# Kernel tuning notes

Hardware: AMD Instinct MI355X
Metric: run time of the kernel (lower is better)

## Reference

```python
import jax, jax.numpy as jnp
import numpy as np

B, DM, H, W = 2, 96, 48, 48
E = 192          # d_expand == d_inner
R, N = 6, 16     # delta_rank, d_state


def conv2d(x, w, b, groups=1, pad=0):
    out = jax.lax.conv_general_dilated(
        x, w, window_strides=(1, 1), padding=[(pad, pad), (pad, pad)],
        dimension_numbers=("NCHW", "OIHW", "NCHW"), feature_group_count=groups)
    return out + b[None, :, None, None]


def setup_inputs() -> dict:
    key = jax.random.key(0)
    ks = jax.random.split(key, 24)
    f = lambda k, shape, s: jax.random.normal(k, shape, jnp.float32) * s
    inp = {
        "x": jax.random.normal(ks[0], (B, DM, H, W), jnp.float32),
        "in_proj_w": f(ks[1], (2 * E, DM), 0.05),
        "conv_w": f(ks[2], (E, 1, 3, 3), 0.2),
        "conv_b": f(ks[3], (E,), 0.1),
        "x_proj_w": f(ks[4], (4, R + 2 * N, E), 0.01),
        "dt_proj_w": f(ks[5], (4, E, R), 0.01),
        "dt_proj_b": jnp.full((4, E), -9.0) + f(ks[6], (4, E), 0.1),
        "A_log": jnp.tile(jnp.log(jnp.arange(1, N + 1, dtype=jnp.float32))[None, None, :], (4, E, 1)),
        "Ds": jnp.ones((4, E), jnp.float32),
        "ln_g": jnp.ones(E, jnp.float32), "ln_b": jnp.zeros(E, jnp.float32),
        "c1_w": f(ks[7], (2 * E, E, 1, 1), 0.05), "c1_b": jnp.zeros(2 * E),
        "bn1_g": jnp.ones(2 * E), "bn1_b": jnp.zeros(2 * E), "bn1_m": jnp.zeros(2 * E), "bn1_v": jnp.ones(2 * E),
        "c2_w": f(ks[8], (2 * E, 1, 3, 3), 0.2), "c2_b": jnp.zeros(2 * E),
        "bn2_g": jnp.ones(2 * E), "bn2_b": jnp.zeros(2 * E), "bn2_m": jnp.zeros(2 * E), "bn2_v": jnp.ones(2 * E),
        "c3_w": f(ks[9], (E // 2, 2 * E, 1, 1), 0.05), "c3_b": jnp.zeros(E // 2),
        "se1_w": f(ks[10], (E // 4, E // 2), 0.1), "se1_b": jnp.zeros(E // 4),
        "se2_w": f(ks[11], (E // 2, E // 4), 0.1), "se2_b": jnp.zeros(E // 2),
    }
    return inp


def reference(x, in_proj_w, conv_w, conv_b, x_proj_w, dt_proj_w, dt_proj_b,
              A_log, Ds, ln_g, ln_b,
              c1_w, c1_b, bn1_g, bn1_b, bn1_m, bn1_v,
              c2_w, c2_b, bn2_g, bn2_b, bn2_m, bn2_v,
              c3_w, c3_b, se1_w, se1_b, se2_w, se2_b):
    Bs, _, Hs, Ws = x.shape
    L = Hs * Ws
    # in projection (Linear over channel dim), split x/z gates
    xz = jnp.einsum("bchw,oc->bohw", x, in_proj_w)
    xi, z = jnp.split(xz, 2, axis=1)
    # depthwise conv + SiLU
    xi = jax.nn.silu(conv2d(xi, conv_w, conv_b, groups=E, pad=1))
    # ---- selective scan (4-direction cross scan, cumsum formulation) ----
    xf = xi.reshape(Bs, E, L)
    xt = jnp.swapaxes(xi, 2, 3).reshape(Bs, E, L)
    xs = jnp.stack([xf, xf[..., ::-1], xt, xt[..., ::-1]], axis=1)  # [B,4,E,L]
    dbc = jnp.einsum("bkcl,krc->bkrl", xs, x_proj_w)                # [B,4,R+2N,L]
    dlt, b, c = dbc[:, :, :R], dbc[:, :, R:R + N], dbc[:, :, R + N:]
    dlt = jnp.einsum("bkrl,kdr->bkdl", dlt, dt_proj_w) + dt_proj_b[None, :, :, None]
    dlt = jax.nn.softplus(dlt)                                      # [B,4,E,L]
    dA = dlt[..., None] * A_log[None, :, :, None, :]                # [B,4,E,L,N]
    phi = jnp.exp(-jnp.cumsum(dA, axis=3))
    dbx = dlt[..., None] * jnp.swapaxes(b, 2, 3)[:, :, None] * xs[..., None]  # [B,4,E,L,N]
    h = phi * jnp.cumsum(dbx / (phi + 1e-12), axis=3)
    y = jnp.einsum("bkdln,bknl->bkdl", h, c) + Ds[None, :, :, None]  # [B,4,E,L]
    # ---- cross merge ----
    y1 = y[:, 0]
    y2 = y[:, 1, :, ::-1]
    y3 = jnp.swapaxes(y[:, 2].reshape(Bs, E, Ws, Hs), 2, 3).reshape(Bs, E, L)
    y4 = jnp.swapaxes(y[:, 3, :, ::-1].reshape(Bs, E, Ws, Hs), 2, 3).reshape(Bs, E, L)
    ys = (y1 + y2 + y3 + y4).reshape(Bs, E, Hs, Ws)
    # layernorm over channels
    yn = jnp.moveaxis(ys, 1, -1)
    mu = yn.mean(-1, keepdims=True)
    var = yn.var(-1, keepdims=True)
    yn = (yn - mu) / jnp.sqrt(var + 1e-5) * ln_g + ln_b
    u = jnp.moveaxis(yn, -1, 1) * z
    # ---- EFFN ----
    def bn(t, g, bb, m, v):
        return (t - m[None, :, None, None]) / jnp.sqrt(v + 1e-5)[None, :, None, None] * g[None, :, None, None] + bb[None, :, None, None]
    t = jax.nn.relu(bn(conv2d(u, c1_w, c1_b), bn1_g, bn1_b, bn1_m, bn1_v))
    t = jax.nn.relu(bn(conv2d(t, c2_w, c2_b, groups=2 * E, pad=1), bn2_g, bn2_b, bn2_m, bn2_v))
    t = conv2d(t, c3_w, c3_b)
    # squeeze-excitation: t + t * sigmoid(fc(relu(fc(avgpool(t)))))
    s = t.mean((2, 3))
    s = jax.nn.relu(s @ se1_w.T + se1_b)
    s = jax.nn.sigmoid(s @ se2_w.T + se2_b)
    return t + t * s[:, :, None, None]
```

## Files before the change

kernel.cpp:

```cpp
#include <hip/hip_runtime.h>
#include <hip/hip_bf16.h>

#define LTOT 2304
#define ECH  192
#define NCH  16
#define CCH  192
#define SCH  12

__device__ __forceinline__ int permS(int k, int l) {
  if (k == 0) return l;
  if (k == 1) return LTOT - 1 - l;
  int m = (k == 2) ? l : (LTOT - 1 - l);
  return (m % 48) * 48 + (m / 48);
}

__device__ __forceinline__ float sp_fast(float x) {
  float t = __expf(x);
  return (t <= 0.018f) ? t * fmaf(t, fmaf(t, 0.33333334f, -0.5f), 1.f) : log1pf(t);
}

__global__ __launch_bounds__(256) void k1_inproj(const float* __restrict__ x,
                                                 const float* __restrict__ W,
                                                 float* __restrict__ xi_pre,
                                                 float* __restrict__ z) {
  const int l0 = blockIdx.x * 32;
  const int o0 = blockIdx.y * 64;
  const int b  = blockIdx.z;
  __shared__ __align__(16) float xs[96 * 34];
  __shared__ __align__(16) float Wl[96 * 68];
  const int tid = threadIdx.x;
  for (int idx = tid; idx < 96 * 32; idx += 256) {
    int i = idx & 31, cc = idx >> 5;
    xs[cc * 34 + i] = x[(b * 96 + cc) * LTOT + l0 + i];
  }
  for (int idx = tid; idx < 64 * 96; idx += 256) {
    int r = idx / 96, cc = idx - r * 96;
    Wl[cc * 68 + r] = W[(o0 + r) * 96 + cc];
  }
  __syncthreads();
  const int lane = tid & 63, w = tid >> 6;
  const int jj = lane & 15, rqq = lane >> 4;
  const int rbase = 16 * w + 4 * rqq;
  float acc[2][4];
#pragma unroll
  for (int p = 0; p < 2; ++p)
#pragma unroll
    for (int t = 0; t < 4; ++t) acc[p][t] = 0.f;
#pragma unroll 4
  for (int cc = 0; cc < 96; ++cc) {
    const float4 wv = *(const float4*)&Wl[cc * 68 + rbase];
    const float2 xv = *(const float2*)&xs[cc * 34 + 2 * jj];
    acc[0][0] = fmaf(wv.x, xv.x, acc[0][0]); acc[0][1] = fmaf(wv.y, xv.x, acc[0][1]);
    acc[0][2] = fmaf(wv.z, xv.x, acc[0][2]); acc[0][3] = fmaf(wv.w, xv.x, acc[0][3]);
    acc[1][0] = fmaf(wv.x, xv.y, acc[1][0]); acc[1][1] = fmaf(wv.y, xv.y, acc[1][1]);
    acc[1][2] = fmaf(wv.z, xv.y, acc[1][2]); acc[1][3] = fmaf(wv.w, xv.y, acc[1][3]);
  }
  __syncthreads();
  float* ol = xs;
#pragma unroll
  for (int t = 0; t < 4; ++t) {
    ol[(rbase + t) * 33 + 2 * jj]     = acc[0][t];
    ol[(rbase + t) * 33 + 2 * jj + 1] = acc[1][t];
  }
  __syncthreads();
  for (int idx = tid; idx < 32 * 64; idx += 256) {
    int r = idx & 63, pos = idx >> 6;
    float v = ol[r * 33 + pos];
    int o = o0 + r, l = l0 + pos;
    if (o < ECH) xi_pre[(b * LTOT + l) * ECH + o] = v;
    else         z[(b * LTOT + l) * ECH + (o - ECH)] = v;
  }
}

__global__ __launch_bounds__(256) void k2_dwconv(const float* __restrict__ xi_pre,
                                                 const float* __restrict__ cw,
                                                 const float* __restrict__ cb,
                                                 float* __restrict__ xi) {
  int g = blockIdx.x * 256 + threadIdx.x;
  if (g >= 2 * LTOT * ECH) return;
  int e = g % ECH; int l = (g / ECH) % LTOT; int b = g / (ECH * LTOT);
  int h = l / 48, wq = l % 48;
  float acc = cb[e];
#pragma unroll
  for (int kh = 0; kh < 3; ++kh) {
    int hh = h + kh - 1; if (hh < 0 || hh >= 48) continue;
#pragma unroll
    for (int kw = 0; kw < 3; ++kw) {
      int ww = wq + kw - 1; if (ww < 0 || ww >= 48) continue;
      acc = fmaf(cw[e * 9 + kh * 3 + kw], xi_pre[(b * LTOT + hh * 48 + ww) * ECH + e], acc);
    }
  }
  xi[g] = acc / (1.f + __expf(-acc));
}

__global__ __launch_bounds__(256) void k3_xproj(const float* __restrict__ xi,
                                                const float* __restrict__ xw,
                                                float* __restrict__ dl6g,
                                                float* __restrict__ bT,
                                                float* __restrict__ cT) {
  const int l0 = blockIdx.x * 32;
  const int k  = blockIdx.y;
  const int b  = blockIdx.z;
  __shared__ __align__(16) float xs[96 * 34];
  __shared__ __align__(16) float Wl[192 * 40];
  const int tid = threadIdx.x;
  const float* wsrc = xw + k * 38 * ECH;
  for (int idx = tid; idx < 38 * 192; idx += 256) {
    int r = idx / 192, cc = idx - r * 192;
    Wl[cc * 40 + r] = wsrc[idx];
  }
  const int lane = tid & 63, w = tid >> 6;
  const int jj = lane & 15;
  const int rq = w * 4 + (lane >> 4);
  const int rqc = rq < 9 ? rq : 9;
  const int j0 = 2 * jj;
  float a00 = 0.f, a01 = 0.f, a02 = 0.f, a03 = 0.f;
  float a10 = 0.f, a11 = 0.f, a12 = 0.f, a13 = 0.f;
  for (int kc = 0; kc < 2; ++kc) {
    __syncthreads();
    for (int idx = tid; idx < 32 * 96; idx += 256) {
      int j = idx / 96, cc = idx - j * 96;
      int s = permS(k, l0 + j);
      xs[cc * 34 + j] = xi[(b * LTOT + s) * ECH + kc * 96 + cc];
    }
    __syncthreads();
#pragma unroll 4
    for (int cc = 0; cc < 96; ++cc) {
      const float2 xv = *(const float2*)&xs[cc * 34 + j0];
      const float4 wv = *(const float4*)&Wl[(kc * 96 + cc) * 40 + 4 * rqc];
      a00 = fmaf(wv.x, xv.x, a00); a01 = fmaf(wv.y, xv.x, a01);
      a02 = fmaf(wv.z, xv.x, a02); a03 = fmaf(wv.w, xv.x, a03);
      a10 = fmaf(wv.x, xv.y, a10); a11 = fmaf(wv.y, xv.y, a11);
      a12 = fmaf(wv.z, xv.y, a12); a13 = fmaf(wv.w, xv.y, a13);
    }
  }
  const int bk = b * 4 + k;
  if (rq < 10) {
    float av[2][4] = {{a00, a01, a02, a03}, {a10, a11, a12, a13}};
#pragma unroll
    for (int t = 0; t < 4; ++t) {
      int r = 4 * rq + t;
      if (r >= 38) continue;
#pragma unroll
      for (int p = 0; p < 2; ++p) {
        int j = j0 + p;
        float v = av[p][t];
        if (r < 6)       dl6g[((bk * LTOT) + l0 + j) * 6 + r] = v;
        else if (r < 22) bT[((bk * LTOT) + l0 + j) * NCH + (r - 6)] = v;
        else             cT[((bk * LTOT) + l0 + j) * NCH + (r - 22)] = v;
      }
    }
  }
}

__global__ __launch_bounds__(256) void k4a_scan1(const float* __restrict__ dl6g,
                                                 const float* __restrict__ xi,
                                                 const float* __restrict__ bT,
                                                 const float* __restrict__ Alog,
                                                 const float* __restrict__ dtw,
                                                 const float* __restrict__ dtb,
                                                 float* __restrict__ q,
                                                 float* __restrict__ Ts) {
  const int cb = blockIdx.x;
  const int db = blockIdx.y;
  const int bk = blockIdx.z;
  const int b = bk >> 2, k = bk & 3;
  const int l0 = cb * 48;
  __shared__ __align__(16) float2 sdx[48 * 64];
  __shared__ __align__(16) float  sb[48 * NCH];
  const int tid = threadIdx.x;
  const int dd = tid & 63, cg = tid >> 6;
  const int dg = db * 64 + dd;
  float b6 = dtb[k * ECH + dg];
  float w6[6];
  {
    const float2* d2 = (const float2*)(dtw + (k * ECH + dg) * 6);
    float2 u0 = d2[0], u1 = d2[1], u2 = d2[2];
    w6[0] = u0.x; w6[1] = u0.y; w6[2] = u1.x; w6[3] = u1.y; w6[4] = u2.x; w6[5] = u2.y;
  }
  for (int idx = tid; idx < 48 * NCH; idx += 256) sb[idx] = bT[(bk * LTOT + l0) * NCH + idx];
  for (int e = tid; e < 48 * 64; e += 256) {
    int s = e >> 6;
    const float* d6 = dl6g + (bk * LTOT + l0 + s) * 6;
    float xa = b6;
#pragma unroll
    for (int r = 0; r < 6; ++r) xa = fmaf(w6[r], d6[r], xa);
    float dl = sp_fast(xa);
    int sp = permS(k, l0 + s);
    sdx[s * 64 + dd] = make_float2(dl, xi[(b * LTOT + sp) * ECH + dg]);
  }
  float C1[16], h[16];
#pragma unroll
  for (int n = 0; n < 16; ++n) {
    C1[n] = Alog[(k * ECH + dg) * NCH + n];
    h[n] = 0.f;
  }
  __syncthreads();
  float Tsum = 0.f;
  for (int i = 0; i < SCH; ++i) {
    int j = cg * SCH + i;
    float2 dx = sdx[j * 64 + dd];
    float dl = dx.x;
    float u  = dl * dx.y;
    Tsum += dl;
    const float4* bb4 = (const float4*)(sb + j * NCH);
    float4 q0 = bb4[0], q1 = bb4[1], q2 = bb4[2], q3 = bb4[3];
    float bbl[16] = {q0.x, q0.y, q0.z, q0.w, q1.x, q1.y, q1.z, q1.w,
                     q2.x, q2.y, q2.z, q2.w, q3.x, q3.y, q3.z, q3.w};
    if (dl <= 0.018f) {
#pragma unroll
      for (int n = 0; n < 16; ++n) {
        float xn = C1[n] * dl;
        float e = fmaf(xn, fmaf(xn, fmaf(xn, -(1.f / 6.f), 0.5f), -1.f), 1.f);
        h[n] = fmaf(e, h[n], u * bbl[n]);
      }
    } else {
#pragma unroll
      for (int n = 0; n < 16; ++n) {
        float e = __expf(-C1[n] * dl);
        h[n] = fmaf(e, h[n], u * bbl[n]);
      }
    }
  }
  const int c = cb * 4 + cg;
  float4* qp = (float4*)(q + ((bk * CCH + c) * ECH + dg) * NCH);
  qp[0] = make_float4(h[0], h[1], h[2], h[3]);
  qp[1] = make_float4(h[4], h[5], h[6], h[7]);
  qp[2] = make_float4(h[8], h[9], h[10], h[11]);
  qp[3] = make_float4(h[12], h[13], h[14], h[15]);
  Ts[(bk * CCH + c) * ECH + dg] = Tsum;
}

__global__ __launch_bounds__(256) void k4b_comb(const float* __restrict__ Alog,
                                                const float* __restrict__ Ts,
                                                float* __restrict__ q) {
  const int d  = blockIdx.x;
  const int bk = blockIdx.y;
  const int k  = bk & 3;
  const int tid = threadIdx.x;
  const int n = tid & 15, seg = tid >> 4;
  const float A = Alog[(k * ECH + d) * NCH + n];
  const int c0 = seg * 12;
  const float* tb = Ts + (bk * CCH + c0) * ECH + d;
  float* qp = q + ((bk * CCH + c0) * ECH + d) * NCH + n;
  float qv[12], P[12];
#pragma unroll
  for (int i = 0; i < 12; ++i) qv[i] = qp[i * (ECH * NCH)];
#pragma unroll
  for (int i = 0; i < 12; ++i) {
    float xv = A * tb[i * ECH];
    P[i] = (xv <= 0.05f)
               ? fmaf(xv, fmaf(xv, fmaf(xv, -(1.f / 6.f), 0.5f), -1.f), 1.f)
               : __expf(-xv);
  }
  float hl = 0.f, Pp = 1.f;
#pragma unroll
  for (int i = 0; i < 12; ++i) { hl = fmaf(P[i], hl, qv[i]); Pp *= P[i]; }
  __shared__ float2 comb[16][17];
  comb[seg][n] = make_float2(Pp, hl);
  __syncthreads();
  float H = 0.f;
  for (int s = 0; s < seg; ++s) {
    float2 cb = comb[s][n];
    H = fmaf(cb.x, H, cb.y);
  }
  float h = H;
#pragma unroll
  for (int i = 0; i < 12; ++i) {
    float hp = h;
    h = fmaf(P[i], h, qv[i]);
    qp[i * (ECH * NCH)] = hp;
  }
}

__global__ __launch_bounds__(256) void k4c_scan2(const float* __restrict__ dl6g,
                                                 const float* __restrict__ xi,
                                                 const float* __restrict__ bT,
                                                 const float* __restrict__ cT,
                                                 const float* __restrict__ Alog,
                                                 const float* __restrict__ dtw,
                                                 const float* __restrict__ dtb,
                                                 const float* __restrict__ hin,
                                                 float* __restrict__ yd) {
  const int cb = blockIdx.x;
  const int db = blockIdx.y;
  const int bk = blockIdx.z;
  const int b = bk >> 2, k = bk & 3;
  const int l0 = cb * 48;
  __shared__ __align__(16) float2 sdx[48 * 64];
  __shared__ __align__(16) float  sb[48 * NCH];
  __shared__ __align__(16) float  sc[48 * NCH];
  const int tid = threadIdx.x;
  const int dd = tid & 63, cg = tid >> 6;
  const int dg = db * 64 + dd;
  float b6 = dtb[k * ECH + dg];
  float w6[6];
  {
    const float2* d2 = (const float2*)(dtw + (k * ECH + dg) * 6);
    float2 u0 = d2[0], u1 = d2[1], u2 = d2[2];
    w6[0] = u0.x; w6[1] = u0.y; w6[2] = u1.x; w6[3] = u1.y; w6[4] = u2.x; w6[5] = u2.y;
  }
  for (int idx = tid; idx < 48 * NCH; idx += 256) {
    sb[idx] = bT[(bk * LTOT + l0) * NCH + idx];
    sc[idx] = cT[(bk * LTOT + l0) * NCH + idx];
  }
  for (int e = tid; e < 48 * 64; e += 256) {
    int s = e >> 6;
    const float* d6 = dl6g + (bk * LTOT + l0 + s) * 6;
    float xa = b6;
#pragma unroll
    for (int r = 0; r < 6; ++r) xa = fmaf(w6[r], d6[r], xa);
    float dl = sp_fast(xa);
    int sp = permS(k, l0 + s);
    sdx[s * 64 + dd] = make_float2(dl, xi[(b * LTOT + sp) * ECH + dg]);
  }
  float C1[16], h[16];
  const int c = cb * 4 + cg;
  const float4* hp = (const float4*)(hin + ((bk * CCH + c) * ECH + dg) * NCH);
  {
    float4 h0 = hp[0], h1 = hp[1], h2 = hp[2], h3 = hp[3];
    h[0]=h0.x; h[1]=h0.y; h[2]=h0.z; h[3]=h0.w;
    h[4]=h1.x; h[5]=h1.y; h[6]=h1.z; h[7]=h1.w;
    h[8]=h2.x; h[9]=h2.y; h[10]=h2.z; h[11]=h2.w;
    h[12]=h3.x; h[13]=h3.y; h[14]=h3.z; h[15]=h3.w;
  }
#pragma unroll
  for (int n = 0; n < 16; ++n) C1[n] = Alog[(k * ECH + dg) * NCH + n];
  float* ydk = yd + (b * 4 + k) * LTOT * ECH;
  __syncthreads();
  for (int i = 0; i < SCH; ++i) {
    int j = cg * SCH + i;
    float2 dx = sdx[j * 64 + dd];
    float dl = dx.x;
    float u  = dl * dx.y;
    const float4* bb4 = (const float4*)(sb + j * NCH);
    float4 q0 = bb4[0], q1 = bb4[1], q2 = bb4[2], q3 = bb4[3];
    float bbl[16] = {q0.x, q0.y, q0.z, q0.w, q1.x, q1.y, q1.z, q1.w,
                     q2.x, q2.y, q2.z, q2.w, q3.x, q3.y, q3.z, q3.w};
    if (dl <= 0.018f) {
#pragma unroll
      for (int n = 0; n < 16; ++n) {
        float xn = C1[n] * dl;
        float e = fmaf(xn, fmaf(xn, fmaf(xn, -(1.f / 6.f), 0.5f), -1.f), 1.f);
        h[n] = fmaf(e, h[n], u * bbl[n]);
      }
    } else {
#pragma unroll
      for (int n = 0; n < 16; ++n) {
        float e = __expf(-C1[n] * dl);
        h[n] = fmaf(e, h[n], u * bbl[n]);
      }
    }
    const float4* cc4 = (const float4*)(sc + j * NCH);
    float4 c0 = cc4[0], c1 = cc4[1], c2 = cc4[2], c3 = cc4[3];
    float ccl[16] = {c0.x, c0.y, c0.z, c0.w, c1.x, c1.y, c1.z, c1.w,
                     c2.x, c2.y, c2.z, c2.w, c3.x, c3.y, c3.z, c3.w};
    float y = 0.f;
#pragma unroll
    for (int n = 0; n < 16; ++n) y = fmaf(h[n], ccl[n], y);
    int sp = permS(k, l0 + j);
    ydk[sp * ECH + dg] = y;
  }
}

__global__ __launch_bounds__(256) void k5_ln(const float* __restrict__ yd,
                                             const float* __restrict__ Ds,
                                             const float* __restrict__ lng,
                                             const float* __restrict__ lnb,
                                             float* __restrict__ zu) {
  int p = blockIdx.x * 4 + (threadIdx.x >> 6);
  int lane = threadIdx.x & 63;
  int b = (p >= LTOT) ? 1 : 0;
  int l = p - b * LTOT;
  const float* y0 = yd + (b * 4) * LTOT * ECH + l * ECH;
  float vd[3], sd[3];
#pragma unroll
  for (int t = 0; t < 3; ++t) {
    int d = lane + t * 64;
    vd[t] = ((y0[d] + y0[LTOT * ECH + d]) + y0[2 * LTOT * ECH + d]) + y0[3 * LTOT * ECH + d];
    sd[t] = Ds[d] + Ds[ECH + d] + Ds[2 * ECH + d] + Ds[3 * ECH + d];
  }
  float s1 = vd[0] + vd[1] + vd[2];
  float s2 = sd[0] + sd[1] + sd[2];
#pragma unroll
  for (int off = 32; off > 0; off >>= 1) {
    s1 += __shfl_xor(s1, off, 64);
    s2 += __shfl_xor(s2, off, 64);
  }
  float mean_dot = s1 * (1.f / 192.f);
  float mean_sd  = s2 * (1.f / 192.f);
  float dev[3];
  float ss = 0.f;
#pragma unroll
  for (int t = 0; t < 3; ++t) {
    dev[t] = (vd[t] - mean_dot) + (sd[t] - mean_sd);
    ss = fmaf(dev[t], dev[t], ss);
  }
#pragma unroll
  for (int off = 32; off > 0; off >>= 1) ss += __shfl_xor(ss, off, 64);
  float rstd = 1.f / sqrtf(ss * (1.f / 192.f) + 1e-5f);
#pragma unroll
  for (int t = 0; t < 3; ++t) {
    int d = lane + t * 64;
    float yn = (dev[t] * rstd) * lng[d] + lnb[d];
    zu[p * ECH + d] = yn * zu[p * ECH + d];
  }
}

__global__ __launch_bounds__(256) void k6_c1(const float* __restrict__ u,
                                             const float* __restrict__ W,
                                             const float* __restrict__ c1b,
                                             const float* __restrict__ g1,
                                             const float* __restrict__ b1,
                                             const float* __restrict__ m1,
                                             const float* __restrict__ v1,
                                             float* __restrict__ t1,
                                             float* __restrict__ se) {
  const int l0 = blockIdx.x * 32;
  const int o0 = blockIdx.y * 64;
  const int b  = blockIdx.z;
  const int tid = threadIdx.x;
  if (blockIdx.x == 0 && blockIdx.y == 0 && blockIdx.z == 0 && tid < 192) se[tid] = 0.f;
  __shared__ __align__(16) float xs[96 * 34];
  __shared__ __align__(16) float Wl[96 * 68];
  const int lane = tid & 63, w = tid >> 6;
  const int jj = lane & 15, rqq = lane >> 4;
  const int rbase = 16 * w + 4 * rqq;
  float acc[2][4];
#pragma unroll
  for (int p = 0; p < 2; ++p)
#pragma unroll
    for (int t = 0; t < 4; ++t) acc[p][t] = 0.f;
  for (int kc = 0; kc < 2; ++kc) {
    if (kc) __syncthreads();
    for (int idx = tid; idx < 32 * 96; idx += 256) {
      int cc = idx % 96, i = idx / 96;
      xs[cc * 34 + i] = u[(b * LTOT + l0 + i) * ECH + kc * 96 + cc];
    }
    for (int idx = tid; idx < 64 * 96; idx += 256) {
      int r = idx / 96, cc = idx - r * 96;
      Wl[cc * 68 + r] = W[(o0 + r) * ECH + kc * 96 + cc];
    }
    __syncthreads();
#pragma unroll 4
    for (int cc = 0; cc < 96; ++cc) {
      const float4 wv = *(const float4*)&Wl[cc * 68 + rbase];
      const float2 xv = *(const float2*)&xs[cc * 34 + 2 * jj];
      acc[0][0] = fmaf(wv.x, xv.x, acc[0][0]); acc[0][1] = fmaf(wv.y, xv.x, acc[0][1]);
      acc[0][2] = fmaf(wv.z, xv.x, acc[0][2]); acc[0][3] = fmaf(wv.w, xv.x, acc[0][3]);
      acc[1][0] = fmaf(wv.x, xv.y, acc[1][0]); acc[1][1] = fmaf(wv.y, xv.y, acc[1][1]);
      acc[1][2] = fmaf(wv.z, xv.y, acc[1][2]); acc[1][3] = fmaf(wv.w, xv.y, acc[1][3]);
    }
  }
#pragma unroll
  for (int t = 0; t < 4; ++t) {
    int o = o0 + rbase + t;
    float sc = g1[o] / sqrtf(v1[o] + 1e-5f);
    float bias = (c1b[o] - m1[o]) * sc + b1[o];
#pragma unroll
    for (int p = 0; p < 2; ++p) acc[p][t] = fmaxf(fmaf(acc[p][t], sc, bias), 0.f);
  }
  __syncthreads();
  float* ol = xs;
#pragma unroll
  for (int t = 0; t < 4; ++t) {
    ol[(rbase + t) * 33 + 2 * jj]     = acc[0][t];
    ol[(rbase + t) * 33 + 2 * jj + 1] = acc[1][t];
  }
  __syncthreads();
  for (int idx = tid; idx < 32 * 64; idx += 256) {
    int pos = idx & 31, r = idx >> 5;
    t1[(b * 384 + o0 + r) * LTOT + l0 + pos] = ol[r * 33 + pos];
  }
}

__global__ __launch_bounds__(256) void k7_dw2(const float* __restrict__ t1,
                                              const float* __restrict__ cw,
                                              const float* __restrict__ cb,
                                              const float* __restrict__ g2,
                                              const float* __restrict__ b2,
                                              const float* __restrict__ m2,
                                              const float* __restrict__ v2,
                                              float* __restrict__ t2) {
  int g = blockIdx.x * 256 + threadIdx.x;
  if (g >= 2 * LTOT * 384) return;
  int l = g % LTOT; int o = (g / LTOT) % 384; int b = g / (LTOT * 384);
  int h = l / 48, wq = l % 48;
  const float* src = t1 + (b * 384 + o) * LTOT;
  float acc = cb[o];
#pragma unroll
  for (int kh = 0; kh < 3; ++kh) {
    int hh = h + kh - 1; if (hh < 0 || hh >= 48) continue;
#pragma unroll
    for (int kw = 0; kw < 3; ++kw) {
      int ww = wq + kw - 1; if (ww < 0 || ww >= 48) continue;
      acc = fmaf(cw[o * 9 + kh * 3 + kw], src[hh * 48 + ww], acc);
    }
  }
  float sc = g2[o] / sqrtf(v2[o] + 1e-5f);
  float val = (acc - m2[o]) * sc + b2[o];
  t2[g] = fmaxf(val, 0.f);
}

__global__ __launch_bounds__(256) void k8_c3(const float* __restrict__ t2,
                                             const float* __restrict__ W,
                                             const float* __restrict__ c3b,
                                             float* __restrict__ t3,
                                             float* __restrict__ se) {
  const int l0 = blockIdx.x * 32;
  const int r0 = blockIdx.y * 32;
  const int b  = blockIdx.z;
  __shared__ __align__(16) float Wl[384 * 34];
  __shared__ __align__(16) float xs[192 * 34];
  const int tid = threadIdx.x;
  const int lane = tid & 63, w = tid >> 6;
  const int jj = lane & 15, rqq = lane >> 4;
  const int rloc = 8 * w + 2 * rqq;
  for (int idx = tid; idx < 32 * 384; idx += 256) {
    int r = idx / 384, cc = idx - r * 384;
    Wl[cc * 34 + r] = W[(r0 + r) * 384 + cc];
  }
  float acc[2][2];
  acc[0][0] = acc[0][1] = acc[1][0] = acc[1][1] = 0.f;
  for (int kc = 0; kc < 2; ++kc) {
    if (kc) __syncthreads();
    for (int idx = tid; idx < 192 * 32; idx += 256) {
      int i = idx & 31, cc = idx >> 5;
      xs[cc * 34 + i] = t2[(b * 384 + kc * 192 + cc) * LTOT + l0 + i];
    }
    __syncthreads();
#pragma unroll 4
    for (int cc = 0; cc < 192; ++cc) {
      const float2 wv = *(const float2*)&Wl[(kc * 192 + cc) * 34 + rloc];
      const float2 xv = *(const float2*)&xs[cc * 34 + 2 * jj];
      acc[0][0] = fmaf(wv.x, xv.x, acc[0][0]); acc[0][1] = fmaf(wv.y, xv.x, acc[0][1]);
      acc[1][0] = fmaf(wv.x, xv.y, acc[1][0]); acc[1][1] = fmaf(wv.y, xv.y, acc[1][1]);
    }
  }
  {
    float b0 = c3b[r0 + rloc], b1v = c3b[r0 + rloc + 1];
    acc[0][0] += b0; acc[1][0] += b0; acc[0][1] += b1v; acc[1][1] += b1v;
  }
#pragma unroll
  for (int t = 0; t < 2; ++t) {
    float v = acc[0][t] + acc[1][t];
    v += __shfl_xor(v, 1); v += __shfl_xor(v, 2);
    v += __shfl_xor(v, 4); v += __shfl_xor(v, 8);
    if (jj == 0) atomicAdd(&se[b * 96 + r0 + rloc + t], v);
  }
  __syncthreads();
  float* ol = xs;
#pragma unroll
  for (int t = 0; t < 2; ++t) {
    ol[(rloc + t) * 33 + 2 * jj]     = acc[0][t];
    ol[(rloc + t) * 33 + 2 * jj + 1] = acc[1][t];
  }
  __syncthreads();
  for (int idx = tid; idx < 32 * 32; idx += 256) {
    int pos = idx & 31, r = idx >> 5;
    t3[(b * 96 + r0 + r) * LTOT + l0 + pos] = ol[r * 33 + pos];
  }
}

__global__ __launch_bounds__(256) void k9_out(const float* __restrict__ t3,
                                              const float* __restrict__ se,
                                              const float* __restrict__ w1,
                                              const float* __restrict__ sb1,
                                              const float* __restrict__ w2,
                                              const float* __restrict__ sb2,
                                              float* __restrict__ out) {
  __shared__ float sm[192];
  __shared__ float s1[96];
  __shared__ float smul[192];
  int t = threadIdx.x;
  if (t < 192) sm[t] = se[t] * (1.f / 2304.f);
  __syncthreads();
  if (t < 96) {
    int b = t / 48, i = t % 48;
    float a = sb1[i];
#pragma unroll 4
    for (int m = 0; m < 96; ++m) a = fmaf(w1[i * 96 + m], sm[b * 96 + m], a);
    s1[t] = fmaxf(a, 0.f);
  }
  __syncthreads();
  if (t < 192) {
    int b = t / 96, j = t % 96;
    float a = sb2[j];
#pragma unroll 4
    for (int i = 0; i < 48; ++i) a = fmaf(w2[j * 48 + i], s1[b * 48 + i], a);
    smul[t] = 1.f + 1.f / (1.f + __expf(-a));
  }
  __syncthreads();
  int g = blockIdx.x * 256 + t;
  if (g < 2 * 96 * LTOT) out[g] = t3[g] * smul[g / LTOT];
}

extern "C" void kernel_launch(void* const* d_in, const int* in_sizes, int n_in,
                              void* d_out, int out_size, void* d_ws, size_t ws_size,
                              hipStream_t stream) {
  const float* x     = (const float*)d_in[0];
  const float* inw   = (const float*)d_in[1];
  const float* convw = (const float*)d_in[2];
  const float* convb = (const float*)d_in[3];
  const float* xpw   = (const float*)d_in[4];
  const float* dtw   = (const float*)d_in[5];
  const float* dtb   = (const float*)d_in[6];
  const float* Alog  = (const float*)d_in[7];
  const float* Ds    = (const float*)d_in[8];
  const float* lng   = (const float*)d_in[9];
  const float* lnb   = (const float*)d_in[10];
  const float* c1w   = (const float*)d_in[11];
  const float* c1b   = (const float*)d_in[12];
  const float* bn1g  = (const float*)d_in[13];
  const float* bn1b  = (const float*)d_in[14];
  const float* bn1m  = (const float*)d_in[15];
  const float* bn1v  = (const float*)d_in[16];
  const float* c2w   = (const float*)d_in[17];
  const float* c2b   = (const float*)d_in[18];
  const float* bn2g  = (const float*)d_in[19];
  const float* bn2b  = (const float*)d_in[20];
  const float* bn2m  = (const float*)d_in[21];
  const float* bn2v  = (const float*)d_in[22];
  const float* c3w   = (const float*)d_in[23];
  const float* c3b   = (const float*)d_in[24];
  const float* se1w  = (const float*)d_in[25];
  const float* se1b  = (const float*)d_in[26];
  const float* se2w  = (const float*)d_in[27];
  const float* se2b  = (const float*)d_in[28];

  float* ws = (float*)d_ws;
  float* xi_pre = ws;
  float* z      = ws + 884736;
  float* xi     = ws + 1769472;
  float* dl6g   = ws + 2654208;
  float* bT     = ws + 2764800;
  float* cT     = ws + 3354624;
  float* q      = ws + 3944448;
  float* Ts     = ws + 13381632;
  float* se     = ws + 13676544;
  float* yd     = ws + 13676736;
  float* t1 = yd;
  float* t2 = yd + 1769472;
  float* t3 = q;

  k1_inproj<<<dim3(72, 6, 2), 256, 0, stream>>>(x, inw, xi_pre, z);
  k2_dwconv<<<3456, 256, 0, stream>>>(xi_pre, convw, convb, xi);
  k3_xproj<<<dim3(72, 4, 2), 256, 0, stream>>>(xi, xpw, dl6g, bT, cT);
  k4a_scan1<<<dim3(48, 3, 8), 256, 0, stream>>>(dl6g, xi, bT, Alog, dtw, dtb, q, Ts);
  k4b_comb<<<dim3(192, 8), 256, 0, stream>>>(Alog, Ts, q);
  k4c_scan2<<<dim3(48, 3, 8), 256, 0, stream>>>(dl6g, xi, bT, cT, Alog, dtw, dtb, q, yd);
  k5_ln<<<1152, 256, 0, stream>>>(yd, Ds, lng, lnb, z);
  k6_c1<<<dim3(72, 6, 2), 256, 0, stream>>>(z, c1w, c1b, bn1g, bn1b, bn1m, bn1v, t1, se);
  k7_dw2<<<6912, 256, 0, stream>>>(t1, c2w, c2b, bn2g, bn2b, bn2m, bn2v, t2);
  k8_c3<<<dim3(72, 3, 2), 256, 0, stream>>>(t2, c3w, c3b, t3, se);
  k9_out<<<1728, 256, 0, stream>>>(t3, se, se1w, se1b, se2w, se2b, (float*)d_out);
}
```

Baseline: 301.0 us.

## Vectorize dwconvs, atomically merge scan directions, and premultiply delta*x in scan

The change makes the depthwise convolutions in k2 and k7 compute four outputs per thread with float4 loads and stores, with the weights hoisted into registers. k4c now accumulates the four scan directions into one zeroed buffer through atomicAdd, so k5 reads one tensor instead of four, at the cost of atomic traffic plus an extra memset. It also precomputes delta*x when staging to shared memory, vectorizes the weight transpose loads in k1 and k6, and pads k3's weight stride in shared memory. The atomic float adds make the summation order nondeterministic, and the workspace aliases for t1, t2 and t3 are moved into the q region.

```diff
diff --git a/kernel.cpp b/kernel.cpp
--- a/kernel.cpp
+++ b/kernel.cpp
@@ -33,9 +33,14 @@
     int i = idx & 31, cc = idx >> 5;
     xs[cc * 34 + i] = x[(b * 96 + cc) * LTOT + l0 + i];
   }
-  for (int idx = tid; idx < 64 * 96; idx += 256) {
-    int r = idx / 96, cc = idx - r * 96;
-    Wl[cc * 68 + r] = W[(o0 + r) * 96 + cc];
+  for (int idx = tid; idx < 96 * 16; idx += 256) {
+    int cc = idx % 96, rq = idx / 96;
+    float4 v;
+    v.x = W[(o0 + 4 * rq + 0) * 96 + cc];
+    v.y = W[(o0 + 4 * rq + 1) * 96 + cc];
+    v.z = W[(o0 + 4 * rq + 2) * 96 + cc];
+    v.w = W[(o0 + 4 * rq + 3) * 96 + cc];
+    *(float4*)&Wl[cc * 68 + 4 * rq] = v;
   }
   __syncthreads();
   const int lane = tid & 63, w = tid >> 6;
@@ -72,25 +77,40 @@
   }
 }
 
-__global__ __launch_bounds__(256) void k2_dwconv(const float* __restrict__ xi_pre,
+__global__ __launch_bounds__(256) void k2_dwconv(const float4* __restrict__ xi_pre4,
                                                  const float* __restrict__ cw,
                                                  const float* __restrict__ cb,
-                                                 float* __restrict__ xi) {
+                                                 float4* __restrict__ xi4) {
   int g = blockIdx.x * 256 + threadIdx.x;
-  if (g >= 2 * LTOT * ECH) return;
-  int e = g % ECH; int l = (g / ECH) % LTOT; int b = g / (ECH * LTOT);
+  if (g >= 2 * LTOT * 48) return;
+  int e4 = g % 48; int l = (g / 48) % LTOT; int b = g / (48 * LTOT);
   int h = l / 48, wq = l % 48;
-  float acc = cb[e];
+  int e0 = 4 * e4;
+  float wt[4][9];
+#pragma unroll
+  for (int j = 0; j < 4; ++j)
+#pragma unroll
+    for (int t = 0; t < 9; ++t) wt[j][t] = cw[(e0 + j) * 9 + t];
+  float4 acc = *(const float4*)&cb[e0];
 #pragma unroll
   for (int kh = 0; kh < 3; ++kh) {
     int hh = h + kh - 1; if (hh < 0 || hh >= 48) continue;
 #pragma unroll
     for (int kw = 0; kw < 3; ++kw) {
       int ww = wq + kw - 1; if (ww < 0 || ww >= 48) continue;
-      acc = fmaf(cw[e * 9 + kh * 3 + kw], xi_pre[(b * LTOT + hh * 48 + ww) * ECH + e], acc);
-    }
-  }
-  xi[g] = acc / (1.f + __expf(-acc));
+      float4 v = xi_pre4[(b * LTOT + hh * 48 + ww) * 48 + e4];
+      int t = kh * 3 + kw;
+      acc.x = fmaf(wt[0][t], v.x, acc.x);
+      acc.y = fmaf(wt[1][t], v.y, acc.y);
+      acc.z = fmaf(wt[2][t], v.z, acc.z);
+      acc.w = fmaf(wt[3][t], v.w, acc.w);
+    }
+  }
+  acc.x = acc.x / (1.f + __expf(-acc.x));
+  acc.y = acc.y / (1.f + __expf(-acc.y));
+  acc.z = acc.z / (1.f + __expf(-acc.z));
+  acc.w = acc.w / (1.f + __expf(-acc.w));
+  xi4[g] = acc;
 }
 
 __global__ __launch_bounds__(256) void k3_xproj(const float* __restrict__ xi,
@@ -102,12 +122,12 @@
   const int k  = blockIdx.y;
   const int b  = blockIdx.z;
   __shared__ __align__(16) float xs[96 * 34];
-  __shared__ __align__(16) float Wl[192 * 40];
+  __shared__ __align__(16) float Wl[192 * 44];
   const int tid = threadIdx.x;
   const float* wsrc = xw + k * 38 * ECH;
   for (int idx = tid; idx < 38 * 192; idx += 256) {
     int r = idx / 192, cc = idx - r * 192;
-    Wl[cc * 40 + r] = wsrc[idx];
+    Wl[cc * 44 + r] = wsrc[idx];
   }
   const int lane = tid & 63, w = tid >> 6;
   const int jj = lane & 15;
@@ -127,7 +147,7 @@
 #pragma unroll 4
     for (int cc = 0; cc < 96; ++cc) {
       const float2 xv = *(const float2*)&xs[cc * 34 + j0];
-      const float4 wv = *(const float4*)&Wl[(kc * 96 + cc) * 40 + 4 * rqc];
+      const float4 wv = *(const float4*)&Wl[(kc * 96 + cc) * 44 + 4 * rqc];
       a00 = fmaf(wv.x, xv.x, a00); a01 = fmaf(wv.y, xv.x, a01);
       a02 = fmaf(wv.z, xv.x, a02); a03 = fmaf(wv.w, xv.x, a03);
       a10 = fmaf(wv.x, xv.y, a10); a11 = fmaf(wv.y, xv.y, a11);
@@ -187,7 +207,7 @@
     for (int r = 0; r < 6; ++r) xa = fmaf(w6[r], d6[r], xa);
     float dl = sp_fast(xa);
     int sp = permS(k, l0 + s);
-    sdx[s * 64 + dd] = make_float2(dl, xi[(b * LTOT + sp) * ECH + dg]);
+    sdx[s * 64 + dd] = make_float2(dl, dl * xi[(b * LTOT + sp) * ECH + dg]);
   }
   float C1[16], h[16];
 #pragma unroll
@@ -201,7 +221,7 @@
     int j = cg * SCH + i;
     float2 dx = sdx[j * 64 + dd];
     float dl = dx.x;
-    float u  = dl * dx.y;
+    float u  = dx.y;
     Tsum += dl;
     const float4* bb4 = (const float4*)(sb + j * NCH);
     float4 q0 = bb4[0], q1 = bb4[1], q2 = bb4[2], q3 = bb4[3];
@@ -281,7 +301,7 @@
                                                  const float* __restrict__ dtw,
                                                  const float* __restrict__ dtb,
                                                  const float* __restrict__ hin,
-                                                 float* __restrict__ yd) {
+                                                 float* __restrict__ ys) {
   const int cb = blockIdx.x;
   const int db = blockIdx.y;
   const int bk = blockIdx.z;
@@ -312,7 +332,7 @@
     for (int r = 0; r < 6; ++r) xa = fmaf(w6[r], d6[r], xa);
     float dl = sp_fast(xa);
     int sp = permS(k, l0 + s);
-    sdx[s * 64 + dd] = make_float2(dl, xi[(b * LTOT + sp) * ECH + dg]);
+    sdx[s * 64 + dd] = make_float2(dl, dl * xi[(b * LTOT + sp) * ECH + dg]);
   }
   float C1[16], h[16];
   const int c = cb * 4 + cg;
@@ -326,13 +346,12 @@
   }
 #pragma unroll
   for (int n = 0; n < 16; ++n) C1[n] = Alog[(k * ECH + dg) * NCH + n];
-  float* ydk = yd + (b * 4 + k) * LTOT * ECH;
   __syncthreads();
   for (int i = 0; i < SCH; ++i) {
     int j = cg * SCH + i;
     float2 dx = sdx[j * 64 + dd];
     float dl = dx.x;
-    float u  = dl * dx.y;
+    float u  = dx.y;
     const float4* bb4 = (const float4*)(sb + j * NCH);
     float4 q0 = bb4[0], q1 = bb4[1], q2 = bb4[2], q3 = bb4[3];
     float bbl[16] = {q0.x, q0.y, q0.z, q0.w, q1.x, q1.y, q1.z, q1.w,
@@ -359,25 +378,23 @@
 #pragma unroll
     for (int n = 0; n < 16; ++n) y = fmaf(h[n], ccl[n], y);
     int sp = permS(k, l0 + j);
-    ydk[sp * ECH + dg] = y;
-  }
-}
-
-__global__ __launch_bounds__(256) void k5_ln(const float* __restrict__ yd,
+    atomicAdd(&ys[(b * LTOT + sp) * ECH + dg], y);
+  }
+}
+
+__global__ __launch_bounds__(256) void k5_ln(const float* __restrict__ ys,
                                              const float* __restrict__ Ds,
                                              const float* __restrict__ lng,
                                              const float* __restrict__ lnb,
                                              float* __restrict__ zu) {
   int p = blockIdx.x * 4 + (threadIdx.x >> 6);
   int lane = threadIdx.x & 63;
-  int b = (p >= LTOT) ? 1 : 0;
-  int l = p - b * LTOT;
-  const float* y0 = yd + (b * 4) * LTOT * ECH + l * ECH;
+  const float* yp = ys + p * ECH;
   float vd[3], sd[3];
 #pragma unroll
   for (int t = 0; t < 3; ++t) {
     int d = lane + t * 64;
-    vd[t] = ((y0[d] + y0[LTOT * ECH + d]) + y0[2 * LTOT * ECH + d]) + y0[3 * LTOT * ECH + d];
+    vd[t] = yp[d];
     sd[t] = Ds[d] + Ds[ECH + d] + Ds[2 * ECH + d] + Ds[3 * ECH + d];
   }
   float s1 = vd[0] + vd[1] + vd[2];
@@ -437,9 +454,14 @@
       int cc = idx % 96, i = idx / 96;
       xs[cc * 34 + i] = u[(b * LTOT + l0 + i) * ECH + kc * 96 + cc];
     }
-    for (int idx = tid; idx < 64 * 96; idx += 256) {
-      int r = idx / 96, cc = idx - r * 96;
-      Wl[cc * 68 + r] = W[(o0 + r) * ECH + kc * 96 + cc];
+    for (int idx = tid; idx < 96 * 16; idx += 256) {
+      int cc = idx % 96, rq = idx / 96;
+      float4 v;
+      v.x = W[(o0 + 4 * rq + 0) * ECH + kc * 96 + cc];
+      v.y = W[(o0 + 4 * rq + 1) * ECH + kc * 96 + cc];
+      v.z = W[(o0 + 4 * rq + 2) * ECH + kc * 96 + cc];
+      v.w = W[(o0 + 4 * rq + 3) * ECH + kc * 96 + cc];
+      *(float4*)&Wl[cc * 68 + 4 * rq] = v;
     }
     __syncthreads();
 #pragma unroll 4
@@ -483,23 +505,35 @@
                                               const float* __restrict__ v2,
                                               float* __restrict__ t2) {
   int g = blockIdx.x * 256 + threadIdx.x;
-  if (g >= 2 * LTOT * 384) return;
-  int l = g % LTOT; int o = (g / LTOT) % 384; int b = g / (LTOT * 384);
-  int h = l / 48, wq = l % 48;
+  if (g >= 2 * 384 * 576) return;
+  int p = g % 576; int o = (g / 576) % 384; int b = g / (576 * 384);
+  int l0 = 4 * p; int h = l0 / 48; int wq0 = l0 % 48;
   const float* src = t1 + (b * 384 + o) * LTOT;
-  float acc = cb[o];
+  float wt[9];
+#pragma unroll
+  for (int t = 0; t < 9; ++t) wt[t] = cw[o * 9 + t];
+  float bias0 = cb[o];
+  float4 a = make_float4(bias0, bias0, bias0, bias0);
 #pragma unroll
   for (int kh = 0; kh < 3; ++kh) {
     int hh = h + kh - 1; if (hh < 0 || hh >= 48) continue;
-#pragma unroll
-    for (int kw = 0; kw < 3; ++kw) {
-      int ww = wq + kw - 1; if (ww < 0 || ww >= 48) continue;
-      acc = fmaf(cw[o * 9 + kh * 3 + kw], src[hh * 48 + ww], acc);
-    }
+    const float* row = src + hh * 48;
+    float4 c = *(const float4*)(row + wq0);
+    float lft = (wq0 > 0)  ? row[wq0 - 1] : 0.f;
+    float rgt = (wq0 < 44) ? row[wq0 + 4] : 0.f;
+    float w0 = wt[kh * 3], w1 = wt[kh * 3 + 1], w2 = wt[kh * 3 + 2];
+    a.x = fmaf(w0, lft, fmaf(w1, c.x, fmaf(w2, c.y, a.x)));
+    a.y = fmaf(w0, c.x, fmaf(w1, c.y, fmaf(w2, c.z, a.y)));
+    a.z = fmaf(w0, c.y, fmaf(w1, c.z, fmaf(w2, c.w, a.z)));
+    a.w = fmaf(w0, c.z, fmaf(w1, c.w, fmaf(w2, rgt, a.w)));
   }
   float sc = g2[o] / sqrtf(v2[o] + 1e-5f);
-  float val = (acc - m2[o]) * sc + b2[o];
-  t2[g] = fmaxf(val, 0.f);
+  float bs = (0.f - m2[o]) * sc + b2[o];
+  a.x = fmaxf(fmaf(a.x, sc, bs), 0.f);
+  a.y = fmaxf(fmaf(a.y, sc, bs), 0.f);
+  a.z = fmaxf(fmaf(a.z, sc, bs), 0.f);
+  a.w = fmaxf(fmaf(a.w, sc, bs), 0.f);
+  *(float4*)(t2 + (b * 384 + o) * LTOT + l0) = a;
 }
 
 __global__ __launch_bounds__(256) void k8_c3(const float* __restrict__ t2,
@@ -638,20 +672,22 @@
   float* q      = ws + 3944448;
   float* Ts     = ws + 13381632;
   float* se     = ws + 13676544;
-  float* yd     = ws + 13676736;
-  float* t1 = yd;
-  float* t2 = yd + 1769472;
-  float* t3 = q;
+  float* ys     = ws + 13676736;
+  float* t1 = q;
+  float* t2 = q + 1769472;
+  float* t3 = q + 3538944;
+
+  hipMemsetAsync(ys, 0, 884736 * sizeof(float), stream);
 
   k1_inproj<<<dim3(72, 6, 2), 256, 0, stream>>>(x, inw, xi_pre, z);
-  k2_dwconv<<<3456, 256, 0, stream>>>(xi_pre, convw, convb, xi);
+  k2_dwconv<<<864, 256, 0, stream>>>((const float4*)xi_pre, convw, convb, (float4*)xi);
   k3_xproj<<<dim3(72, 4, 2), 256, 0, stream>>>(xi, xpw, dl6g, bT, cT);
   k4a_scan1<<<dim3(48, 3, 8), 256, 0, stream>>>(dl6g, xi, bT, Alog, dtw, dtb, q, Ts);
   k4b_comb<<<dim3(192, 8), 256, 0, stream>>>(Alog, Ts, q);
-  k4c_scan2<<<dim3(48, 3, 8), 256, 0, stream>>>(dl6g, xi, bT, cT, Alog, dtw, dtb, q, yd);
-  k5_ln<<<1152, 256, 0, stream>>>(yd, Ds, lng, lnb, z);
+  k4c_scan2<<<dim3(48, 3, 8), 256, 0, stream>>>(dl6g, xi, bT, cT, Alog, dtw, dtb, q, ys);
+  k5_ln<<<1152, 256, 0, stream>>>(ys, Ds, lng, lnb, z);
   k6_c1<<<dim3(72, 6, 2), 256, 0, stream>>>(z, c1w, c1b, bn1g, bn1b, bn1m, bn1v, t1, se);
-  k7_dw2<<<6912, 256, 0, stream>>>(t1, c2w, c2b, bn2g, bn2b, bn2m, bn2v, t2);
+  k7_dw2<<<1728, 256, 0, stream>>>(t1, c2w, c2b, bn2g, bn2b, bn2m, bn2v, t2);
   k8_c3<<<dim3(72, 3, 2), 256, 0, stream>>>(t2, c3w, c3b, t3, se);
   k9_out<<<1728, 256, 0, stream>>>(t3, se, se1w, se1b, se2w, se2b, (float*)d_out);
 }
```

New measurement: 291.7 us. -3.1%, faster.
